# Performance work log

Measured on AMD Instinct MI355X. Metric: run time of the kernel, lower is better.

## Reference

```python
import jax, jax.numpy as jnp
import numpy as np


def setup_inputs() -> dict:
    key = jax.random.key(0)
    k1, k2 = jax.random.split(key)
    B, N, M = 4, 16384, 4096
    src_points = jax.random.normal(k1, (B, N, 3), dtype=jnp.float32)
    target_verts = jax.random.normal(k2, (B, M, 3), dtype=jnp.float32)
    return {"src_points": src_points, "target_verts": target_verts}


def reference(src_points, target_verts):
    # target_faces=None path of ChamferLoss: degenerate one-vertex triangles,
    # so closest-point-on-mesh == nearest target vertex.
    # d2[b,n,m] = ||p_bn - v_bm||^2 via the expansion p2 + v2 - 2 p.v
    p2 = jnp.sum(src_points * src_points, axis=-1)          # (B, N)
    v2 = jnp.sum(target_verts * target_verts, axis=-1)      # (B, M)
    pv = jnp.einsum('bnd,bmd->bnm', src_points, target_verts)  # (B, N, M)
    d2 = p2[:, :, None] + v2[:, None, :] - 2.0 * pv
    d2 = jnp.maximum(d2, 0.0)
    min_d2 = jnp.min(d2, axis=-1)                            # (B, N)
    num_src_per_batch = src_points.shape[1]
    loss = jnp.sum(min_d2, axis=-1) / num_src_per_batch      # (B,)
    return loss
```

## Files before the change

### kernel.cpp

```cpp
#include <hip/hip_runtime.h>
#include <float.h>


typedef __bf16 bf16x8 __attribute__((ext_vector_type(8)));
typedef float  f32x16 __attribute__((ext_vector_type(16)));

constexpr int B = 4, N = 16384, M = 4096;
constexpr int BN = B * N;
constexpr int CHUNK_V = 2048;
constexpr int NCHUNK = M / CHUNK_V;
constexpr int TILES = CHUNK_V / 32;
constexpr int TPB = 256;
constexpr int PPB = 256;
constexpr int PBLK = BN / PPB;
constexpr size_t BFRAG_BYTES = (size_t)B * M * 32;

__global__ __launch_bounds__(256) void chamfer_pre(
    const float* __restrict__ tv, unsigned char* __restrict__ bfr,
    float* __restrict__ out)
{
    if (blockIdx.x == 0 && threadIdx.x < B) out[threadIdx.x] = 0.0f;
    int i = blockIdx.x * 256 + threadIdx.x;
    int b = i >> 12;
    int m = i & (M - 1);
    float x = tv[3 * i + 0], y = tv[3 * i + 1], z = tv[3 * i + 2];
    __bf16 xh = (__bf16)x, yh = (__bf16)y, zh = (__bf16)z;
    float xhf = (float)xh, yhf = (float)yh, zhf = (float)zh;
    __bf16 xl = (__bf16)(x - xhf), yl = (__bf16)(y - yhf), zl = (__bf16)(z - zhf);
    float v2 = fmaf(x, x, fmaf(y, y, z * z));
    __bf16 v2h = (__bf16)v2;
    __bf16 v2l = (__bf16)(v2 - (float)v2h);
    __bf16 zero = (__bf16)0.0f;

    bf16x8 h0, h1;
    h0[0] = (__bf16)(-2.0f * xhf); h0[1] = (__bf16)(-2.0f * yhf);
    h0[2] = (__bf16)(-2.0f * zhf);
    h0[3] = h0[0]; h0[4] = h0[1]; h0[5] = h0[2];
    h0[6] = (__bf16)(-2.0f * (float)xl); h0[7] = (__bf16)(-2.0f * (float)yl);
    h1[0] = (__bf16)(-2.0f * (float)zl); h1[1] = v2h; h1[2] = v2l;
    h1[3] = zero; h1[4] = zero; h1[5] = zero; h1[6] = zero; h1[7] = zero;

    int chunk = m >> 11, local = m & 2047, tile = local >> 5, c = m & 31;
    size_t base = (size_t)b * 131072 + (size_t)chunk * 65536 + tile * 1024 + c * 16;
    *(bf16x8*)(bfr + base)       = h0;
    *(bf16x8*)(bfr + base + 512) = h1;
}

__global__ __launch_bounds__(TPB) void chamfer_mfma(
    const float* __restrict__ src, const unsigned char* __restrict__ bfr,
    float* __restrict__ partial)
{
    __shared__ uint4 lds4[4096];
    char* ldsc = (char*)lds4;
    const int blk   = blockIdx.x;
    const int chunk = blk & 1;
    const int pblk  = blk >> 1;
    const int b     = pblk >> 6;
    const int t     = threadIdx.x;
    const int w     = t >> 6, L = t & 63;
    const int half  = L >> 5, c = L & 31;

    const uint4* gsrc = (const uint4*)(bfr + (size_t)b * 131072 + (size_t)chunk * 65536);
#pragma unroll
    for (int i = 0; i < 16; ++i) lds4[i * 256 + t] = gsrc[i * 256 + t];

    const int gpa = pblk * 256 + w * 64 + c;
    const int gpb = gpa + 32;
    float ax = src[3*gpa], ay = src[3*gpa+1], az = src[3*gpa+2];
    float bx = src[3*gpb], by = src[3*gpb+1], bz = src[3*gpb+2];
    __bf16 one = (__bf16)1.0f, zero = (__bf16)0.0f;
    bf16x8 aA, aB;
    {
        __bf16 xh=(__bf16)ax, yh=(__bf16)ay, zh=(__bf16)az;
        __bf16 xl=(__bf16)(ax-(float)xh), yl=(__bf16)(ay-(float)yh), zl=(__bf16)(az-(float)zh);
        if (half == 0) { aA[0]=xh; aA[1]=yh; aA[2]=zh; aA[3]=xl; aA[4]=yl; aA[5]=zl; aA[6]=xh; aA[7]=yh; }
        else { aA[0]=zh; aA[1]=one; aA[2]=one; aA[3]=zero; aA[4]=zero; aA[5]=zero; aA[6]=zero; aA[7]=zero; }
    }
    {
        __bf16 xh=(__bf16)bx, yh=(__bf16)by, zh=(__bf16)bz;
        __bf16 xl=(__bf16)(bx-(float)xh), yl=(__bf16)(by-(float)yh), zl=(__bf16)(bz-(float)zh);
        if (half == 0) { aB[0]=xh; aB[1]=yh; aB[2]=zh; aB[3]=xl; aB[4]=yl; aB[5]=zl; aB[6]=xh; aB[7]=yh; }
        else { aB[0]=zh; aB[1]=one; aB[2]=one; aB[3]=zero; aB[4]=zero; aB[5]=zero; aB[6]=zero; aB[7]=zero; }
    }

    __syncthreads();

    f32x16 mnA, mnB, zeroC;
#pragma unroll
    for (int r = 0; r < 16; ++r) { mnA[r] = FLT_MAX; mnB[r] = FLT_MAX; zeroC[r] = 0.0f; }

    const int laneoff = half * 512 + c * 16;
#pragma unroll 8
    for (int tl = 0; tl < TILES; ++tl) {
        bf16x8 bf = *(const bf16x8*)(ldsc + tl * 1024 + laneoff);
        f32x16 Ca = __builtin_amdgcn_mfma_f32_32x32x16_bf16(aA, bf, zeroC, 0, 0, 0);
        f32x16 Cb = __builtin_amdgcn_mfma_f32_32x32x16_bf16(aB, bf, zeroC, 0, 0, 0);
#pragma unroll
        for (int r = 0; r < 16; ++r) {
            mnA[r] = fminf(mnA[r], Ca[r]);
            mnB[r] = fminf(mnB[r], Cb[r]);
        }
    }

    __syncthreads();

    float* epi = (float*)ldsc;
    const int ta = w * 2, tb = ta + 1;
#pragma unroll
    for (int r = 0; r < 16; ++r) {
        int row = (r & 3) + 8 * (r >> 2) + 4 * half;
        epi[(ta * 32 + row) * 36 + c] = mnA[r];
        epi[(tb * 32 + row) * 36 + c] = mnB[r];
    }
    __syncthreads();

    const float4* rowp = (const float4*)(epi + t * 36);
    float4 q0 = rowp[0], q1 = rowp[1], q2 = rowp[2], q3 = rowp[3];
    float4 q4 = rowp[4], q5 = rowp[5], q6 = rowp[6], q7 = rowp[7];
    float m01 = fminf(fminf(fminf(q0.x,q0.y),fminf(q0.z,q0.w)),
                      fminf(fminf(q1.x,q1.y),fminf(q1.z,q1.w)));
    float m23 = fminf(fminf(fminf(q2.x,q2.y),fminf(q2.z,q2.w)),
                      fminf(fminf(q3.x,q3.y),fminf(q3.z,q3.w)));
    float m45 = fminf(fminf(fminf(q4.x,q4.y),fminf(q4.z,q4.w)),
                      fminf(fminf(q5.x,q5.y),fminf(q5.z,q5.w)));
    float m67 = fminf(fminf(fminf(q6.x,q6.y),fminf(q6.z,q6.w)),
                      fminf(fminf(q7.x,q7.y),fminf(q7.z,q7.w)));
    float mall = fminf(fminf(m01, m23), fminf(m45, m67));
    partial[(size_t)chunk * BN + pblk * 256 + t] = mall;
}

__global__ __launch_bounds__(256) void chamfer_reduce(
    const float* __restrict__ partial, const float* __restrict__ src,
    float* __restrict__ out)
{
    const int p = blockIdx.x * 256 + threadIdx.x;
    const int b = blockIdx.x >> 6;
    float m = fminf(partial[p], partial[(size_t)BN + p]);
    float x = src[3*p], y = src[3*p+1], z = src[3*p+2];
    float pp = fmaf(x, x, fmaf(y, y, z * z));
    float sum = fmaxf(m + pp, 0.0f);

    for (int off = 32; off > 0; off >>= 1)
        sum += __shfl_down(sum, off, 64);
    __shared__ float acc[4];
    if ((threadIdx.x & 63) == 0) acc[threadIdx.x >> 6] = sum;
    __syncthreads();
    if (threadIdx.x == 0) {
        float s = acc[0] + acc[1] + acc[2] + acc[3];
        atomicAdd(&out[b], s * (1.0f / N));
    }
}

extern "C" void kernel_launch(void* const* d_in, const int* in_sizes, int n_in,
                              void* d_out, int out_size, void* d_ws, size_t ws_size,
                              hipStream_t stream) {
    const float* src = (const float*)d_in[0];
    const float* tv  = (const float*)d_in[1];
    float* out = (float*)d_out;
    unsigned char* bfr = (unsigned char*)d_ws;
    float* partial = (float*)((char*)d_ws + BFRAG_BYTES);

    chamfer_pre   <<<(B * M) / 256, 256, 0, stream>>>(tv, bfr, out);
    chamfer_mfma  <<<PBLK * NCHUNK, TPB, 0, stream>>>(src, bfr, partial);
    chamfer_reduce<<<BN / 256, 256, 0, stream>>>(partial, src, out);
}
```

Measured before the change: 74.51 us.

## Read target fragments directly from global memory and split vertices into four chunks

The MFMA kernel no longer stages the 64KB target-fragment chunk in LDS. Each lane now loads its B fragment straight from global memory (through the cache), and the vertex dimension is split into four chunks instead of two, doubling the grid. LDS use drops to a small per-wave epilogue buffer with padded rows, which should allow more blocks per CU and removes the staging copy and a barrier. In exchange the inner loop depends on global/L2 load latency, and the reduce kernel reads twice as much partial data.

```diff
diff --git a/kernel.cpp b/kernel.cpp
--- a/kernel.cpp
+++ b/kernel.cpp
@@ -7,8 +7,8 @@
 
 constexpr int B = 4, N = 16384, M = 4096;
 constexpr int BN = B * N;
-constexpr int CHUNK_V = 2048;
-constexpr int NCHUNK = M / CHUNK_V;
+constexpr int NCHUNK = 4;
+constexpr int CHUNK_V = M / NCHUNK;
 constexpr int TILES = CHUNK_V / 32;
 constexpr int TPB = 256;
 constexpr int PPB = 256;
@@ -40,8 +40,8 @@
     h1[0] = (__bf16)(-2.0f * (float)zl); h1[1] = v2h; h1[2] = v2l;
     h1[3] = zero; h1[4] = zero; h1[5] = zero; h1[6] = zero; h1[7] = zero;
 
-    int chunk = m >> 11, local = m & 2047, tile = local >> 5, c = m & 31;
-    size_t base = (size_t)b * 131072 + (size_t)chunk * 65536 + tile * 1024 + c * 16;
+    int chunk = m >> 10, local = m & (CHUNK_V - 1), tile = local >> 5, c = m & 31;
+    size_t base = (size_t)b * 131072 + (size_t)chunk * 32768 + tile * 1024 + c * 16;
     *(bf16x8*)(bfr + base)       = h0;
     *(bf16x8*)(bfr + base + 512) = h1;
 }
@@ -50,19 +50,14 @@
     const float* __restrict__ src, const unsigned char* __restrict__ bfr,
     float* __restrict__ partial)
 {
-    __shared__ uint4 lds4[4096];
-    char* ldsc = (char*)lds4;
+    __shared__ float epi[4 * 2 * 32 * 33];
     const int blk   = blockIdx.x;
-    const int chunk = blk & 1;
-    const int pblk  = blk >> 1;
+    const int chunk = blk & 3;
+    const int pblk  = blk >> 2;
     const int b     = pblk >> 6;
     const int t     = threadIdx.x;
     const int w     = t >> 6, L = t & 63;
     const int half  = L >> 5, c = L & 31;
-
-    const uint4* gsrc = (const uint4*)(bfr + (size_t)b * 131072 + (size_t)chunk * 65536);
-#pragma unroll
-    for (int i = 0; i < 16; ++i) lds4[i * 256 + t] = gsrc[i * 256 + t];
 
     const int gpa = pblk * 256 + w * 64 + c;
     const int gpb = gpa + 32;
@@ -83,16 +78,15 @@
         else { aB[0]=zh; aB[1]=one; aB[2]=one; aB[3]=zero; aB[4]=zero; aB[5]=zero; aB[6]=zero; aB[7]=zero; }
     }
 
-    __syncthreads();
-
     f32x16 mnA, mnB, zeroC;
 #pragma unroll
     for (int r = 0; r < 16; ++r) { mnA[r] = FLT_MAX; mnB[r] = FLT_MAX; zeroC[r] = 0.0f; }
 
-    const int laneoff = half * 512 + c * 16;
-#pragma unroll 8
+    const char* bp = (const char*)bfr + (size_t)b * 131072
+                   + (size_t)chunk * 32768 + half * 512 + c * 16;
+#pragma unroll 4
     for (int tl = 0; tl < TILES; ++tl) {
-        bf16x8 bf = *(const bf16x8*)(ldsc + tl * 1024 + laneoff);
+        bf16x8 bf = *(const bf16x8*)(bp + (size_t)tl * 1024);
         f32x16 Ca = __builtin_amdgcn_mfma_f32_32x32x16_bf16(aA, bf, zeroC, 0, 0, 0);
         f32x16 Cb = __builtin_amdgcn_mfma_f32_32x32x16_bf16(aB, bf, zeroC, 0, 0, 0);
 #pragma unroll
@@ -102,31 +96,20 @@
         }
     }
 
-    __syncthreads();
-
-    float* epi = (float*)ldsc;
-    const int ta = w * 2, tb = ta + 1;
+    float* epw = epi + w * (2 * 32 * 33);
 #pragma unroll
     for (int r = 0; r < 16; ++r) {
         int row = (r & 3) + 8 * (r >> 2) + 4 * half;
-        epi[(ta * 32 + row) * 36 + c] = mnA[r];
-        epi[(tb * 32 + row) * 36 + c] = mnB[r];
+        epw[row * 33 + c]        = mnA[r];
+        epw[(32 + row) * 33 + c] = mnB[r];
     }
     __syncthreads();
 
-    const float4* rowp = (const float4*)(epi + t * 36);
-    float4 q0 = rowp[0], q1 = rowp[1], q2 = rowp[2], q3 = rowp[3];
-    float4 q4 = rowp[4], q5 = rowp[5], q6 = rowp[6], q7 = rowp[7];
-    float m01 = fminf(fminf(fminf(q0.x,q0.y),fminf(q0.z,q0.w)),
-                      fminf(fminf(q1.x,q1.y),fminf(q1.z,q1.w)));
-    float m23 = fminf(fminf(fminf(q2.x,q2.y),fminf(q2.z,q2.w)),
-                      fminf(fminf(q3.x,q3.y),fminf(q3.z,q3.w)));
-    float m45 = fminf(fminf(fminf(q4.x,q4.y),fminf(q4.z,q4.w)),
-                      fminf(fminf(q5.x,q5.y),fminf(q5.z,q5.w)));
-    float m67 = fminf(fminf(fminf(q6.x,q6.y),fminf(q6.z,q6.w)),
-                      fminf(fminf(q7.x,q7.y),fminf(q7.z,q7.w)));
-    float mall = fminf(fminf(m01, m23), fminf(m45, m67));
-    partial[(size_t)chunk * BN + pblk * 256 + t] = mall;
+    const float* myrow = epi + w * (2 * 32 * 33) + (L >> 5) * (32 * 33) + (L & 31) * 33;
+    float m = myrow[0];
+#pragma unroll
+    for (int k = 1; k < 32; ++k) m = fminf(m, myrow[k]);
+    partial[(size_t)chunk * BN + pblk * 256 + w * 64 + L] = m;
 }
 
 __global__ __launch_bounds__(256) void chamfer_reduce(
@@ -135,7 +118,8 @@
 {
     const int p = blockIdx.x * 256 + threadIdx.x;
     const int b = blockIdx.x >> 6;
-    float m = fminf(partial[p], partial[(size_t)BN + p]);
+    float m = fminf(fminf(partial[p], partial[(size_t)BN + p]),
+                    fminf(partial[2 * (size_t)BN + p], partial[3 * (size_t)BN + p]));
     float x = src[3*p], y = src[3*p+1], z = src[3*p+2];
     float pp = fmaf(x, x, fmaf(y, y, z * z));
     float sum = fmaxf(m + pp, 0.0f);
```

After: 76.05 us. +2.1%, slower.
